# Performance work log

Hardware: AMD Instinct MI355X
Metric: run time of the kernel (lower is better)

The kernel has to match this reference:

```python
import jax, jax.numpy as jnp
import numpy as np

N = 50000      # nodes
E = 800000     # edges
DIN = 128      # input_dim
H = 128        # hidden_dim
DOUT = 64      # output_dim
G = 256        # graphs in batch
HOPS = 2       # num_hops
EPS = 1e-5     # BatchNorm eps


def setup_inputs() -> dict:
    key = jax.random.key(0)
    ks = jax.random.split(key, 16)
    w = lambda k, shape: jax.random.normal(k, shape, jnp.float32) * 0.05
    return dict(
        x=jax.random.normal(ks[0], (N, DIN), jnp.float32),
        edge_index=jax.random.randint(ks[1], (2, E), 0, N),
        batch=jnp.sort(jax.random.randint(ks[2], (N,), 0, G)),
        # preprocess FFNN (weights stored [in, out]; math == torch x @ W.T + b)
        pre_w1=w(ks[3], (DIN, H)), pre_b1=jnp.zeros((H,), jnp.float32),
        pre_w2=w(ks[4], (H, H)),   pre_b2=jnp.zeros((H,), jnp.float32),
        # per-hop GCNConv weight/bias
        conv_w=w(ks[5], (HOPS, H, H)), conv_b=jnp.zeros((HOPS, H), jnp.float32),
        # per-hop FFNN
        ffnn_w1=w(ks[6], (HOPS, H, H)), ffnn_b1=jnp.zeros((HOPS, H), jnp.float32),
        ffnn_w2=w(ks[7], (HOPS, H, H)), ffnn_b2=jnp.zeros((HOPS, H), jnp.float32),
        # per-hop BatchNorm affine params
        bn_gamma=jnp.ones((HOPS, H), jnp.float32), bn_beta=jnp.zeros((HOPS, H), jnp.float32),
        # postprocess FFNN
        post_w1=w(ks[8], (H, H)),    post_b1=jnp.zeros((H,), jnp.float32),
        post_w2=w(ks[9], (H, DOUT)), post_b2=jnp.zeros((DOUT,), jnp.float32),
    )


def _ffnn(x, w1, b1, w2, b2):
    # Linear -> GELU(exact, erf-based like nn.GELU) -> Linear
    return jax.nn.gelu(x @ w1 + b1, approximate=False) @ w2 + b2


def reference(x, edge_index, batch,
              pre_w1, pre_b1, pre_w2, pre_b2,
              conv_w, conv_b, ffnn_w1, ffnn_b1, ffnn_w2, ffnn_b2,
              bn_gamma, bn_beta,
              post_w1, post_b1, post_w2, post_b2):
    n = x.shape[0]
    loops = jnp.arange(n)
    # GCNConv default: add self-loops, symmetric D^-1/2 A D^-1/2 normalization
    src = jnp.concatenate([edge_index[0], loops])
    dst = jnp.concatenate([edge_index[1], loops])
    deg = jax.ops.segment_sum(jnp.ones(src.shape[0], x.dtype), dst, num_segments=n)
    dis = jnp.where(deg > 0, jax.lax.rsqrt(deg), 0.0)
    norm = dis[src] * dis[dst]  # [E+N]

    x = _ffnn(x, pre_w1, pre_b1, pre_w2, pre_b2)  # preprocess
    for i in range(HOPS):
        # GCNConv: (x W) gathered at src, scaled, scatter-added at dst, + bias
        xw = x @ conv_w[i]
        agg = jax.ops.segment_sum(xw[src] * norm[:, None], dst, num_segments=n) + conv_b[i]
        x = agg + x  # residual
        # BatchNorm1d (training-mode batch statistics, biased variance)
        mean = x.mean(axis=0)
        var = x.var(axis=0)
        x = (x - mean) * jax.lax.rsqrt(var + EPS) * bn_gamma[i] + bn_beta[i]
        # dropout treated as identity (deterministic reference)
        x = _ffnn(x, ffnn_w1[i], ffnn_b1[i], ffnn_w2[i], ffnn_b2[i]) + x
    # global_mean_pool over graph ids
    sums = jax.ops.segment_sum(x, batch, num_segments=G)
    cnt = jax.ops.segment_sum(jnp.ones(n, x.dtype), batch, num_segments=G)
    pooled = sums / jnp.maximum(cnt, 1.0)[:, None]
    return _ffnn(pooled, post_w1, post_b1, post_w2, post_b2)
```

## Files before the change

### kernel.cpp

```cpp
#include <hip/hip_runtime.h>
#include <hip/hip_bf16.h>
#include <math.h>

#define NN 50000
#define EE 800000
#define GG 256

typedef short bf16x8 __attribute__((ext_vector_type(8)));
typedef float f32x4 __attribute__((ext_vector_type(4)));
typedef unsigned int u32x4 __attribute__((ext_vector_type(4)));

__device__ __forceinline__ unsigned short f2bf(float x) {
    __hip_bfloat16 h = __float2bfloat16(x);
    union { __hip_bfloat16 h; unsigned short u; } c; c.h = h; return c.u;
}
__device__ __forceinline__ float bf2f(unsigned short u) {
    union { unsigned int v; float f; } t; t.v = ((unsigned int)u) << 16; return t.f;
}
__device__ __forceinline__ float gelu_f(float v) {
    return 0.5f * v * (1.0f + erff(v * 0.70710678118654752f));
}
__device__ __forceinline__ int swz(int row, int bytecol) {
    return row * 256 + (bytecol ^ ((row & 7) << 4));
}

__global__ void k_deg(const int* __restrict__ dst, int* __restrict__ degi, int E) {
    int i = blockIdx.x * blockDim.x + threadIdx.x;
    if (i < E) atomicAdd(&degi[dst[i]], 1);
}
__global__ void k_scan1(const int* __restrict__ degi, int* __restrict__ incl,
                        int* __restrict__ bsum, int N) {
    __shared__ int sm[1024];
    int t = threadIdx.x, i = blockIdx.x * 1024 + t;
    int v = (i < N) ? degi[i] : 0;
    sm[t] = v;
    __syncthreads();
    for (int off = 1; off < 1024; off <<= 1) {
        int add = (t >= off) ? sm[t - off] : 0;
        __syncthreads();
        sm[t] += add;
        __syncthreads();
    }
    if (i < N) incl[i] = sm[t];
    if (t == 1023) bsum[blockIdx.x] = sm[t];
}
__global__ void k_scan3(const int* __restrict__ incl, const int* __restrict__ degi,
                        const int* __restrict__ bsum, float* __restrict__ dis,
                        int* __restrict__ rowstart, int N, int E, int nsb) {
    __shared__ int sboff;
    int t = threadIdx.x;
    if (t < 64) {
        int nb = blockIdx.x >> 2;
        int v = (t < nb && t < nsb) ? bsum[t] : 0;
        #pragma unroll
        for (int o = 1; o < 64; o <<= 1) v += __shfl_xor(v, o, 64);
        if (t == 0) sboff = v;
    }
    __syncthreads();
    int i = blockIdx.x * 256 + t;
    if (i < N) {
        rowstart[i] = incl[i] - degi[i] + sboff;
        dis[i] = rsqrtf((float)(degi[i] + 1));
    }
    if (i == 0) rowstart[N] = E;
}
__global__ void k_fill(const int* __restrict__ src, const int* __restrict__ dst,
                       const float* __restrict__ dis, const int* __restrict__ rowstart,
                       int* __restrict__ fillc, int* __restrict__ col,
                       float* __restrict__ wn, int E) {
    int i = blockIdx.x * blockDim.x + threadIdx.x;
    if (i < E) {
        int s = src[i], d = dst[i];
        int pos = rowstart[d] + atomicAdd(&fillc[d], 1);
        col[pos] = s;
        wn[pos] = dis[s] * dis[d];
    }
}
__global__ void k_prepw8(const float* __restrict__ w0, const float* __restrict__ w1,
                         const float* __restrict__ w2, const float* __restrict__ w3,
                         const float* __restrict__ w4, const float* __restrict__ w5,
                         const float* __restrict__ w6, const float* __restrict__ w7,
                         unsigned short* __restrict__ Wt) {
    int b = blockIdx.x >> 6;
    const float* W = b == 0 ? w0 : b == 1 ? w1 : b == 2 ? w2 : b == 3 ? w3
                   : b == 4 ? w4 : b == 5 ? w5 : b == 6 ? w6 : w7;
    int tid = (blockIdx.x & 63) * 256 + threadIdx.x;
    int n = tid >> 7, k = tid & 127;
    *(unsigned short*)((char*)(Wt + (size_t)b * 16384) + swz(n, k * 2)) = f2bf(W[k * 128 + n]);
}

__global__ __launch_bounds__(256) void k_mm(
    const float* __restrict__ A32, const unsigned short* __restrict__ A16,
    const unsigned short* __restrict__ W1, const float* __restrict__ b1,
    const unsigned short* __restrict__ W2, const float* __restrict__ b2,
    const unsigned short* __restrict__ W3,
    const float* __restrict__ st_sum, const float* __restrict__ st_sq,
    const float* __restrict__ st_g, const float* __restrict__ st_b,
    float invN, int bn, int hasres,
    float* __restrict__ outx32, unsigned short* __restrict__ out3, int M)
{
    __shared__ unsigned short As[64 * 128];
    __shared__ unsigned short Ws[128 * 128];
    __shared__ float lsc[128], lsh[128];
    const int tid = threadIdx.x;
    const int bm = blockIdx.x * 64;
    if (st_sum && tid < 128) {
        float m = st_sum[tid] * invN;
        float var = st_sq[tid] * invN - m * m;
        float s = st_g[tid] * rsqrtf(var + 1e-5f);
        lsc[tid] = s;
        lsh[tid] = st_b[tid] - m * s;
    }
    __syncthreads();
    {
        const uint4* srcp = (const uint4*)W1;
        uint4* dstp = (uint4*)Ws;
        for (int i = tid; i < 2048; i += 256) dstp[i] = srcp[i];
    }
    #pragma unroll
    for (int pass = 0; pass < 4; ++pass) {
        int row = pass * 16 + (tid >> 4);
        int c8 = tid & 15;
        int gr = bm + row; if (gr > M - 1) gr = M - 1;
        float vv[8];
        if (A32) {
            const float* pp = A32 + (size_t)gr * 128 + c8 * 8;
            float4 v0 = *(const float4*)pp;
            float4 v1 = *(const float4*)(pp + 4);
            vv[0] = v0.x; vv[1] = v0.y; vv[2] = v0.z; vv[3] = v0.w;
            vv[4] = v1.x; vv[5] = v1.y; vv[6] = v1.z; vv[7] = v1.w;
        } else {
            u32x4 raw = __builtin_nontemporal_load((const u32x4*)(A16 + (size_t)gr * 128 + c8 * 8));
            #pragma unroll
            for (int d = 0; d < 4; ++d) {
                vv[2 * d]     = bf2f((unsigned short)(raw[d] & 0xffff));
                vv[2 * d + 1] = bf2f((unsigned short)(raw[d] >> 16));
            }
        }
        if (bn) {
            int ch = c8 * 8;
            #pragma unroll
            for (int j = 0; j < 8; ++j) vv[j] = vv[j] * lsc[ch + j] + lsh[ch + j];
        }
        unsigned short tmp[8];
        #pragma unroll
        for (int j = 0; j < 8; ++j) tmp[j] = f2bf(vv[j]);
        *(uint4*)((char*)As + swz(row, c8 * 16)) = *(uint4*)tmp;
    }
    __syncthreads();

    const int lane = tid & 63, wid = tid >> 6;
    const int r0 = wid * 16;
    const int lrow = lane & 15;
    const int lkb = (lane >> 4) * 16;
    const int cb = lane & 15;
    const int rb = r0 + (lane >> 4) * 4;

    f32x4 acc[8];
    #pragma unroll
    for (int n = 0; n < 8; ++n) acc[n] = (f32x4){0.f, 0.f, 0.f, 0.f};
    #pragma unroll
    for (int kk = 0; kk < 4; ++kk) {
        int bc = kk * 64 + lkb;
        bf16x8 a = *(const bf16x8*)((const char*)As + swz(r0 + lrow, bc));
        #pragma unroll
        for (int n = 0; n < 8; ++n) {
            bf16x8 b = *(const bf16x8*)((const char*)Ws + swz(n * 16 + lrow, bc));
            acc[n] = __builtin_amdgcn_mfma_f32_16x16x32_bf16(a, b, acc[n], 0, 0, 0);
        }
    }
    unsigned short rres[32];
    if (hasres) {
        #pragma unroll
        for (int n = 0; n < 8; ++n)
            #pragma unroll
            for (int j = 0; j < 4; ++j)
                rres[n * 4 + j] = *(const unsigned short*)((const char*)As + swz(rb + j, (n * 16 + cb) * 2));
    }
    #pragma unroll
    for (int n = 0; n < 8; ++n) {
        int colg = n * 16 + cb;
        float bv = b1[colg];
        #pragma unroll
        for (int j = 0; j < 4; ++j) {
            float v = gelu_f(acc[n][j] + bv);
            *(unsigned short*)((char*)As + swz(rb + j, colg * 2)) = f2bf(v);
        }
    }
    __syncthreads();
    {
        const uint4* srcp = (const uint4*)W2;
        uint4* dstp = (uint4*)Ws;
        for (int i = tid; i < 2048; i += 256) dstp[i] = srcp[i];
    }
    __syncthreads();
    #pragma unroll
    for (int n = 0; n < 8; ++n) acc[n] = (f32x4){0.f, 0.f, 0.f, 0.f};
    #pragma unroll
    for (int kk = 0; kk < 4; ++kk) {
        int bc = kk * 64 + lkb;
        bf16x8 a = *(const bf16x8*)((const char*)As + swz(r0 + lrow, bc));
        #pragma unroll
        for (int n = 0; n < 8; ++n) {
            bf16x8 b = *(const bf16x8*)((const char*)Ws + swz(n * 16 + lrow, bc));
            acc[n] = __builtin_amdgcn_mfma_f32_16x16x32_bf16(a, b, acc[n], 0, 0, 0);
        }
    }
    #pragma unroll
    for (int n = 0; n < 8; ++n) {
        int colg = n * 16 + cb;
        float bv = b2[colg];
        #pragma unroll
        for (int j = 0; j < 4; ++j) {
            int rowg = bm + rb + j;
            float v = acc[n][j] + bv;
            if (hasres) v += bf2f(rres[n * 4 + j]);
            if (rowg < M) outx32[(size_t)rowg * 128 + colg] = v;
            if (W3) *(unsigned short*)((char*)As + swz(rb + j, colg * 2)) = f2bf(v);
        }
    }
    if (!W3) return;
    __syncthreads();
    {
        const uint4* srcp = (const uint4*)W3;
        uint4* dstp = (uint4*)Ws;
        for (int i = tid; i < 2048; i += 256) dstp[i] = srcp[i];
    }
    __syncthreads();
    #pragma unroll
    for (int n = 0; n < 8; ++n) acc[n] = (f32x4){0.f, 0.f, 0.f, 0.f};
    #pragma unroll
    for (int kk = 0; kk < 4; ++kk) {
        int bc = kk * 64 + lkb;
        bf16x8 a = *(const bf16x8*)((const char*)As + swz(r0 + lrow, bc));
        #pragma unroll
        for (int n = 0; n < 8; ++n) {
            bf16x8 b = *(const bf16x8*)((const char*)Ws + swz(n * 16 + lrow, bc));
            acc[n] = __builtin_amdgcn_mfma_f32_16x16x32_bf16(a, b, acc[n], 0, 0, 0);
        }
    }
    #pragma unroll
    for (int n = 0; n < 8; ++n) {
        int colg = n * 16 + cb;
        #pragma unroll
        for (int j = 0; j < 4; ++j) {
            int rowg = bm + rb + j;
            if (rowg < M) out3[(size_t)rowg * 128 + colg] = f2bf(acc[n][j]);
        }
    }
}

__global__ __launch_bounds__(256) void k_agg(
    const unsigned short* __restrict__ xw, const int* __restrict__ rowstart,
    const int* __restrict__ col, const float* __restrict__ wn,
    const float* __restrict__ dis, const float* __restrict__ convb,
    const float* __restrict__ x0, unsigned short* __restrict__ zbf,
    float* __restrict__ bnsum, float* __restrict__ bnsq, int N)
{
    __shared__ float redS[4][128];
    __shared__ float redQ[4][128];
    const int tid = threadIdx.x;
    const int lane = tid & 63;
    const int wid = tid >> 6;
    const int g = lane >> 4;
    const int cl = lane & 15;
    const int ch = cl * 8;
    const int wave = blockIdx.x * 4 + wid;
    const int nwaves = gridDim.x * 4;

    float cb[8];
    #pragma unroll
    for (int j = 0; j < 8; ++j) cb[j] = convb[ch + j];
    float s[8], q[8];
    #pragma unroll
    for (int j = 0; j < 8; ++j) { s[j] = 0.f; q[j] = 0.f; }

    for (int v = wave; v < N; v += nwaves) {
        const int e0 = rowstart[v], e1 = rowstart[v + 1];
        float a[8];
        #pragma unroll
        for (int j = 0; j < 8; ++j) a[j] = 0.f;
        int e = e0 + g;
        for (; e + 4 < e1; e += 8) {
            const int u0 = __builtin_nontemporal_load(col + e);
            const float w0 = __builtin_nontemporal_load(wn + e);
            const int u1 = __builtin_nontemporal_load(col + e + 4);
            const float w1 = __builtin_nontemporal_load(wn + e + 4);
            u32x4 p0 = *(const u32x4*)(xw + (size_t)u0 * 128 + ch);
            u32x4 p1 = *(const u32x4*)(xw + (size_t)u1 * 128 + ch);
            #pragma unroll
            for (int d = 0; d < 4; ++d) {
                a[2 * d]     += w0 * bf2f((unsigned short)(p0[d] & 0xffff));
                a[2 * d + 1] += w0 * bf2f((unsigned short)(p0[d] >> 16));
            }
            #pragma unroll
            for (int d = 0; d < 4; ++d) {
                a[2 * d]     += w1 * bf2f((unsigned short)(p1[d] & 0xffff));
                a[2 * d + 1] += w1 * bf2f((unsigned short)(p1[d] >> 16));
            }
        }
        if (e < e1) {
            const int u = __builtin_nontemporal_load(col + e);
            const float w = __builtin_nontemporal_load(wn + e);
            u32x4 p = *(const u32x4*)(xw + (size_t)u * 128 + ch);
            #pragma unroll
            for (int d = 0; d < 4; ++d) {
                a[2 * d]     += w * bf2f((unsigned short)(p[d] & 0xffff));
                a[2 * d + 1] += w * bf2f((unsigned short)(p[d] >> 16));
            }
        }
        #pragma unroll
        for (int j = 0; j < 8; ++j) {
            a[j] += __shfl_xor(a[j], 16, 64);
            a[j] += __shfl_xor(a[j], 32, 64);
        }
        if (g == 0) {
            const float dv = dis[v];
            const float sw = dv * dv;
            u32x4 p = *(const u32x4*)(xw + (size_t)v * 128 + ch);
            f32x4 xa = __builtin_nontemporal_load((const f32x4*)(x0 + (size_t)v * 128 + ch));
            f32x4 xb = __builtin_nontemporal_load((const f32x4*)(x0 + (size_t)v * 128 + ch + 4));
            const float xr[8] = { xa[0], xa[1], xa[2], xa[3], xb[0], xb[1], xb[2], xb[3] };
            float zz[8];
            #pragma unroll
            for (int d = 0; d < 4; ++d) {
                zz[2 * d]     = a[2 * d]     + sw * bf2f((unsigned short)(p[d] & 0xffff));
                zz[2 * d + 1] = a[2 * d + 1] + sw * bf2f((unsigned short)(p[d] >> 16));
            }
            unsigned short zo[8];
            #pragma unroll
            for (int j = 0; j < 8; ++j) {
                zz[j] += cb[j] + xr[j];
                s[j] += zz[j];
                q[j] += zz[j] * zz[j];
                zo[j] = f2bf(zz[j]);
            }
            __builtin_nontemporal_store(*(const u32x4*)zo, (u32x4*)(zbf + (size_t)v * 128 + ch));
        }
    }
    if (g == 0) {
        #pragma unroll
        for (int j = 0; j < 8; ++j) { redS[wid][ch + j] = s[j]; redQ[wid][ch + j] = q[j]; }
    }
    __syncthreads();
    if (tid < 128) {
        float ts = redS[0][tid] + redS[1][tid] + redS[2][tid] + redS[3][tid];
        float tq = redQ[0][tid] + redQ[1][tid] + redQ[2][tid] + redQ[3][tid];
        atomicAdd(&bnsum[tid], ts);
        atomicAdd(&bnsq[tid], tq);
    }
}
__global__ __launch_bounds__(128) void k_pool(
    const float* __restrict__ x, const int* __restrict__ batch,
    float* __restrict__ pooled, int* __restrict__ cnt, int N)
{
    const int t = threadIdx.x;
    const int per = (N + gridDim.x - 1) / gridDim.x;
    const int s = blockIdx.x * per;
    const int e = min(s + per, N);
    if (s >= e) return;
    float acc = 0.f;
    int gcur = batch[s];
    int run = 0;
    for (int v = s; v < e; ++v) {
        int g = batch[v];
        if (g != gcur) {
            atomicAdd(&pooled[(size_t)gcur * 128 + t], acc);
            if (t == 0) atomicAdd(&cnt[gcur], run);
            acc = 0.f; run = 0; gcur = g;
        }
        acc += __builtin_nontemporal_load(x + (size_t)v * 128 + t);
        ++run;
    }
    atomicAdd(&pooled[(size_t)gcur * 128 + t], acc);
    if (t == 0) atomicAdd(&cnt[gcur], run);
}
__global__ __launch_bounds__(128) void k_post(
    const float* __restrict__ pooled, const int* __restrict__ cnt,
    const float* __restrict__ w1, const float* __restrict__ b1,
    const float* __restrict__ w2, const float* __restrict__ b2,
    float* __restrict__ out, int G)
{
    __shared__ float pr[128], hr[128];
    int g = blockIdx.x, t = threadIdx.x;
    float c = fmaxf((float)cnt[g], 1.0f);
    pr[t] = pooled[(size_t)g * 128 + t] / c;
    __syncthreads();
    float a = b1[t];
    for (int k = 0; k < 128; ++k) a += pr[k] * w1[k * 128 + t];
    hr[t] = gelu_f(a);
    __syncthreads();
    if (t < 64) {
        float o = b2[t];
        for (int k = 0; k < 128; ++k) o += hr[k] * w2[k * 64 + t];
        out[g * 64 + t] = o;
    }
}

extern "C" void kernel_launch(void* const* d_in, const int* in_sizes, int n_in,
                              void* d_out, int out_size, void* d_ws, size_t ws_size,
                              hipStream_t stream) {
    (void)in_sizes; (void)n_in; (void)out_size; (void)ws_size;
    const float* x_in    = (const float*)d_in[0];
    const int*   ei      = (const int*)d_in[1];
    const int*   batch   = (const int*)d_in[2];
    const float* pre_w1  = (const float*)d_in[3];
    const float* pre_b1  = (const float*)d_in[4];
    const float* pre_w2  = (const float*)d_in[5];
    const float* pre_b2  = (const float*)d_in[6];
    const float* conv_w  = (const float*)d_in[7];
    const float* conv_b  = (const float*)d_in[8];
    const float* ffnn_w1 = (const float*)d_in[9];
    const float* ffnn_b1 = (const float*)d_in[10];
    const float* ffnn_w2 = (const float*)d_in[11];
    const float* ffnn_b2 = (const float*)d_in[12];
    const float* bn_gamma= (const float*)d_in[13];
    const float* bn_beta = (const float*)d_in[14];
    const float* post_w1 = (const float*)d_in[15];
    const float* post_b1 = (const float*)d_in[16];
    const float* post_w2 = (const float*)d_in[17];
    const float* post_b2 = (const float*)d_in[18];
    const int* srcE = ei;
    const int* dstE = ei + EE;

    char* base = (char*)d_ws;
    size_t off = 0;
    auto carve = [&](size_t bytes) {
        char* q = base + off;
        off = (off + bytes + 255) & ~(size_t)255;
        return q;
    };
    float* xf32 = (float*)carve((size_t)NN * 128 * 4);
    unsigned short* zbf = (unsigned short*)carve((size_t)NN * 128 * 2);
    unsigned short* hbf = (unsigned short*)carve((size_t)NN * 128 * 2);
    float* dis   = (float*)carve((size_t)NN * 4);
    int*   degi  = (int*)carve((size_t)NN * 4);
    int*   fillc = (int*)carve((size_t)NN * 4);
    float* pooled= (float*)carve((size_t)GG * 128 * 4);
    int*   cnt   = (int*)carve((size_t)GG * 4);
    float* bnstat= (float*)carve(512 * 4);
    size_t zlen  = (size_t)((char*)(bnstat + 512) - (char*)degi);
    int* incl    = (int*)carve((size_t)NN * 4);
    int* bsum    = (int*)carve(64 * 4);
    int* rowstart= (int*)carve((size_t)(NN + 1) * 4);
    int* colx    = (int*)carve((size_t)EE * 4);
    float* wn    = (float*)carve((size_t)EE * 4);
    unsigned short* Wt = (unsigned short*)carve((size_t)8 * 16384 * 2);

    hipMemsetAsync(degi, 0, zlen, stream);

    const int nsb = (NN + 1023) / 1024;
    k_deg<<<(EE + 255) / 256, 256, 0, stream>>>(dstE, degi, EE);
    k_scan1<<<nsb, 1024, 0, stream>>>(degi, incl, bsum, NN);
    k_scan3<<<(NN + 255) / 256, 256, 0, stream>>>(incl, degi, bsum, dis, rowstart, NN, EE, nsb);
    k_fill<<<(EE + 255) / 256, 256, 0, stream>>>(srcE, dstE, dis, rowstart, fillc, colx, wn, EE);
    k_prepw8<<<512, 256, 0, stream>>>(pre_w1, pre_w2, conv_w, conv_w + 16384,
                                      ffnn_w1, ffnn_w1 + 16384, ffnn_w2, ffnn_w2 + 16384, Wt);

    const int gB = (NN + 63) / 64;
    const float invN = 1.0f / NN;
    k_mm<<<gB, 256, 0, stream>>>(x_in, nullptr, Wt + 0 * 16384, pre_b1, Wt + 1 * 16384, pre_b2,
                                 Wt + 2 * 16384, nullptr, nullptr, nullptr, nullptr,
                                 invN, 0, 0, xf32, hbf, NN);
    k_agg<<<2048, 256, 0, stream>>>(hbf, rowstart, colx, wn, dis, conv_b,
                                    xf32, zbf, bnstat, bnstat + 128, NN);
    k_mm<<<gB, 256, 0, stream>>>(nullptr, zbf, Wt + 4 * 16384, ffnn_b1, Wt + 6 * 16384, ffnn_b2,
                                 Wt + 3 * 16384, bnstat, bnstat + 128, bn_gamma, bn_beta,
                                 invN, 1, 1, xf32, hbf, NN);
    k_agg<<<2048, 256, 0, stream>>>(hbf, rowstart, colx, wn, dis, conv_b + 128,
                                    xf32, zbf, bnstat + 256, bnstat + 384, NN);
    k_mm<<<gB, 256, 0, stream>>>(nullptr, zbf, Wt + 5 * 16384, ffnn_b1 + 128, Wt + 7 * 16384, ffnn_b2 + 128,
                                 nullptr, bnstat + 256, bnstat + 384, bn_gamma + 128, bn_beta + 128,
                                 invN, 1, 1, xf32, nullptr, NN);
    k_pool<<<1024, 128, 0, stream>>>(xf32, batch, pooled, cnt, NN);
    k_post<<<GG, 128, 0, stream>>>(pooled, cnt, post_w1, post_b1, post_w2, post_b2,
                                   (float*)d_out, GG);
}
```

Measured before the change: 396.6 us.

## Fold GCN normalization into node scaling and fuse mean-pool into final FFNN

The symmetric normalization is refactored: the xW output is pre-scaled by dis[src] in the matmul epilogue and the aggregate is scaled by dis[dst] once per node. This removes the per-edge weight array and its loads, and k_agg gains a 4-way unrolled gather loop. The final FFNN kernel now accumulates graph sums directly into pooled via shared memory and atomics, which drops the fp32 x write and the separate pool kernel. Graph counts come from a binary search over the sorted batch array. The trade-off is bf16 rounding of the pre-scaled values and a dependence on batch being sorted.

```diff
diff --git a/kernel.cpp b/kernel.cpp
--- a/kernel.cpp
+++ b/kernel.cpp
@@ -65,15 +65,13 @@
     if (i == 0) rowstart[N] = E;
 }
 __global__ void k_fill(const int* __restrict__ src, const int* __restrict__ dst,
-                       const float* __restrict__ dis, const int* __restrict__ rowstart,
-                       int* __restrict__ fillc, int* __restrict__ col,
-                       float* __restrict__ wn, int E) {
+                       const int* __restrict__ rowstart,
+                       int* __restrict__ fillc, int* __restrict__ col, int E) {
     int i = blockIdx.x * blockDim.x + threadIdx.x;
     if (i < E) {
         int s = src[i], d = dst[i];
         int pos = rowstart[d] + atomicAdd(&fillc[d], 1);
         col[pos] = s;
-        wn[pos] = dis[s] * dis[d];
     }
 }
 __global__ void k_prepw8(const float* __restrict__ w0, const float* __restrict__ w1,
@@ -93,15 +91,18 @@
     const float* __restrict__ A32, const unsigned short* __restrict__ A16,
     const unsigned short* __restrict__ W1, const float* __restrict__ b1,
     const unsigned short* __restrict__ W2, const float* __restrict__ b2,
-    const unsigned short* __restrict__ W3,
+    const unsigned short* __restrict__ W3, const float* __restrict__ disv,
     const float* __restrict__ st_sum, const float* __restrict__ st_sq,
     const float* __restrict__ st_g, const float* __restrict__ st_b,
     float invN, int bn, int hasres,
-    float* __restrict__ outx32, unsigned short* __restrict__ out3, int M)
+    float* __restrict__ outx32, unsigned short* __restrict__ out3,
+    const int* __restrict__ batch, float* __restrict__ pooled, int M)
 {
     __shared__ unsigned short As[64 * 128];
     __shared__ unsigned short Ws[128 * 128];
     __shared__ float lsc[128], lsh[128];
+    __shared__ float sdis[64];
+    __shared__ int gid[64];
     const int tid = threadIdx.x;
     const int bm = blockIdx.x * 64;
     if (st_sum && tid < 128) {
@@ -206,6 +207,8 @@
             acc[n] = __builtin_amdgcn_mfma_f32_16x16x32_bf16(a, b, acc[n], 0, 0, 0);
         }
     }
+    const int dopool = (pooled != nullptr);
+    float* wsf = (float*)Ws;
     #pragma unroll
     for (int n = 0; n < 8; ++n) {
         int colg = n * 16 + cb;
@@ -215,9 +218,29 @@
             int rowg = bm + rb + j;
             float v = acc[n][j] + bv;
             if (hasres) v += bf2f(rres[n * 4 + j]);
-            if (rowg < M) outx32[(size_t)rowg * 128 + colg] = v;
+            if (outx32 && rowg < M) outx32[(size_t)rowg * 128 + colg] = v;
             if (W3) *(unsigned short*)((char*)As + swz(rb + j, colg * 2)) = f2bf(v);
-        }
+            if (dopool) wsf[(rb + j) * 128 + colg] = v;
+        }
+    }
+    if (dopool) {
+        if (tid < 64) { int r = bm + tid; gid[tid] = (r < M) ? batch[r] : -1; }
+        __syncthreads();
+        if (tid < 128) {
+            float pacc = 0.f;
+            int gcur = gid[0];
+            #pragma unroll 4
+            for (int r = 0; r < 64; ++r) {
+                int gg = gid[r];
+                if (gg != gcur) {
+                    if (gcur >= 0) atomicAdd(&pooled[(size_t)gcur * 128 + tid], pacc);
+                    pacc = 0.f; gcur = gg;
+                }
+                if (gg >= 0) pacc += wsf[r * 128 + tid];
+            }
+            if (gcur >= 0) atomicAdd(&pooled[(size_t)gcur * 128 + tid], pacc);
+        }
+        return;
     }
     if (!W3) return;
     __syncthreads();
@@ -225,6 +248,7 @@
         const uint4* srcp = (const uint4*)W3;
         uint4* dstp = (uint4*)Ws;
         for (int i = tid; i < 2048; i += 256) dstp[i] = srcp[i];
+        if (tid < 64) { int r = bm + tid; sdis[tid] = disv[(r < M) ? r : (M - 1)]; }
     }
     __syncthreads();
     #pragma unroll
@@ -245,14 +269,14 @@
         #pragma unroll
         for (int j = 0; j < 4; ++j) {
             int rowg = bm + rb + j;
-            if (rowg < M) out3[(size_t)rowg * 128 + colg] = f2bf(acc[n][j]);
+            if (rowg < M) out3[(size_t)rowg * 128 + colg] = f2bf(acc[n][j] * sdis[rb + j]);
         }
     }
 }
 
 __global__ __launch_bounds__(256) void k_agg(
-    const unsigned short* __restrict__ xw, const int* __restrict__ rowstart,
-    const int* __restrict__ col, const float* __restrict__ wn,
+    const unsigned short* __restrict__ xws, const int* __restrict__ rowstart,
+    const int* __restrict__ col,
     const float* __restrict__ dis, const float* __restrict__ convb,
     const float* __restrict__ x0, unsigned short* __restrict__ zbf,
     float* __restrict__ bnsum, float* __restrict__ bnsq, int N)
@@ -281,32 +305,41 @@
         #pragma unroll
         for (int j = 0; j < 8; ++j) a[j] = 0.f;
         int e = e0 + g;
+        for (; e + 12 < e1; e += 16) {
+            const int u0 = col[e];
+            const int u1 = col[e + 4];
+            const int u2 = col[e + 8];
+            const int u3 = col[e + 12];
+            u32x4 p0 = *(const u32x4*)(xws + (size_t)u0 * 128 + ch);
+            u32x4 p1 = *(const u32x4*)(xws + (size_t)u1 * 128 + ch);
+            u32x4 p2 = *(const u32x4*)(xws + (size_t)u2 * 128 + ch);
+            u32x4 p3 = *(const u32x4*)(xws + (size_t)u3 * 128 + ch);
+            #pragma unroll
+            for (int d = 0; d < 4; ++d) {
+                a[2 * d]     += bf2f((unsigned short)(p0[d] & 0xffff)) + bf2f((unsigned short)(p1[d] & 0xffff))
+                              + bf2f((unsigned short)(p2[d] & 0xffff)) + bf2f((unsigned short)(p3[d] & 0xffff));
+                a[2 * d + 1] += bf2f((unsigned short)(p0[d] >> 16)) + bf2f((unsigned short)(p1[d] >> 16))
+                              + bf2f((unsigned short)(p2[d] >> 16)) + bf2f((unsigned short)(p3[d] >> 16));
+            }
+        }
         for (; e + 4 < e1; e += 8) {
-            const int u0 = __builtin_nontemporal_load(col + e);
-            const float w0 = __builtin_nontemporal_load(wn + e);
-            const int u1 = __builtin_nontemporal_load(col + e + 4);
-            const float w1 = __builtin_nontemporal_load(wn + e + 4);
-            u32x4 p0 = *(const u32x4*)(xw + (size_t)u0 * 128 + ch);
-            u32x4 p1 = *(const u32x4*)(xw + (size_t)u1 * 128 + ch);
+            const int u0 = col[e];
+            const int u1 = col[e + 4];
+            u32x4 p0 = *(const u32x4*)(xws + (size_t)u0 * 128 + ch);
+            u32x4 p1 = *(const u32x4*)(xws + (size_t)u1 * 128 + ch);
             #pragma unroll
             for (int d = 0; d < 4; ++d) {
-                a[2 * d]     += w0 * bf2f((unsigned short)(p0[d] & 0xffff));
-                a[2 * d + 1] += w0 * bf2f((unsigned short)(p0[d] >> 16));
-            }
+                a[2 * d]     += bf2f((unsigned short)(p0[d] & 0xffff)) + bf2f((unsigned short)(p1[d] & 0xffff));
+                a[2 * d + 1] += bf2f((unsigned short)(p0[d] >> 16)) + bf2f((unsigned short)(p1[d] >> 16));
+            }
+        }
+        if (e < e1) {
+            const int u = col[e];
+            u32x4 p = *(const u32x4*)(xws + (size_t)u * 128 + ch);
             #pragma unroll
             for (int d = 0; d < 4; ++d) {
-                a[2 * d]     += w1 * bf2f((unsigned short)(p1[d] & 0xffff));
-                a[2 * d + 1] += w1 * bf2f((unsigned short)(p1[d] >> 16));
-            }
-        }
-        if (e < e1) {
-            const int u = __builtin_nontemporal_load(col + e);
-            const float w = __builtin_nontemporal_load(wn + e);
-            u32x4 p = *(const u32x4*)(xw + (size_t)u * 128 + ch);
-            #pragma unroll
-            for (int d = 0; d < 4; ++d) {
-                a[2 * d]     += w * bf2f((unsigned short)(p[d] & 0xffff));
-                a[2 * d + 1] += w * bf2f((unsigned short)(p[d] >> 16));
+                a[2 * d]     += bf2f((unsigned short)(p[d] & 0xffff));
+                a[2 * d + 1] += bf2f((unsigned short)(p[d] >> 16));
             }
         }
         #pragma unroll
@@ -316,16 +349,15 @@
         }
         if (g == 0) {
             const float dv = dis[v];
-            const float sw = dv * dv;
-            u32x4 p = *(const u32x4*)(xw + (size_t)v * 128 + ch);
+            u32x4 p = *(const u32x4*)(xws + (size_t)v * 128 + ch);
             f32x4 xa = __builtin_nontemporal_load((const f32x4*)(x0 + (size_t)v * 128 + ch));
             f32x4 xb = __builtin_nontemporal_load((const f32x4*)(x0 + (size_t)v * 128 + ch + 4));
             const float xr[8] = { xa[0], xa[1], xa[2], xa[3], xb[0], xb[1], xb[2], xb[3] };
             float zz[8];
             #pragma unroll
             for (int d = 0; d < 4; ++d) {
-                zz[2 * d]     = a[2 * d]     + sw * bf2f((unsigned short)(p[d] & 0xffff));
-                zz[2 * d + 1] = a[2 * d + 1] + sw * bf2f((unsigned short)(p[d] >> 16));
+                zz[2 * d]     = dv * (a[2 * d]     + bf2f((unsigned short)(p[d] & 0xffff)));
+                zz[2 * d + 1] = dv * (a[2 * d + 1] + bf2f((unsigned short)(p[d] >> 16)));
             }
             unsigned short zo[8];
             #pragma unroll
@@ -350,40 +382,22 @@
         atomicAdd(&bnsq[tid], tq);
     }
 }
-__global__ __launch_bounds__(128) void k_pool(
-    const float* __restrict__ x, const int* __restrict__ batch,
-    float* __restrict__ pooled, int* __restrict__ cnt, int N)
-{
-    const int t = threadIdx.x;
-    const int per = (N + gridDim.x - 1) / gridDim.x;
-    const int s = blockIdx.x * per;
-    const int e = min(s + per, N);
-    if (s >= e) return;
-    float acc = 0.f;
-    int gcur = batch[s];
-    int run = 0;
-    for (int v = s; v < e; ++v) {
-        int g = batch[v];
-        if (g != gcur) {
-            atomicAdd(&pooled[(size_t)gcur * 128 + t], acc);
-            if (t == 0) atomicAdd(&cnt[gcur], run);
-            acc = 0.f; run = 0; gcur = g;
-        }
-        acc += __builtin_nontemporal_load(x + (size_t)v * 128 + t);
-        ++run;
-    }
-    atomicAdd(&pooled[(size_t)gcur * 128 + t], acc);
-    if (t == 0) atomicAdd(&cnt[gcur], run);
-}
 __global__ __launch_bounds__(128) void k_post(
-    const float* __restrict__ pooled, const int* __restrict__ cnt,
+    const float* __restrict__ pooled, const int* __restrict__ batch,
     const float* __restrict__ w1, const float* __restrict__ b1,
     const float* __restrict__ w2, const float* __restrict__ b2,
-    float* __restrict__ out, int G)
+    float* __restrict__ out, int N, int G)
 {
     __shared__ float pr[128], hr[128];
+    __shared__ int bounds[2];
     int g = blockIdx.x, t = threadIdx.x;
-    float c = fmaxf((float)cnt[g], 1.0f);
+    if (t < 2) {
+        int tgt = g + t, lo = 0, hi = N;
+        while (lo < hi) { int mid = (lo + hi) >> 1; if (batch[mid] < tgt) lo = mid + 1; else hi = mid; }
+        bounds[t] = lo;
+    }
+    __syncthreads();
+    float c = fmaxf((float)(bounds[1] - bounds[0]), 1.0f);
     pr[t] = pooled[(size_t)g * 128 + t] / c;
     __syncthreads();
     float a = b1[t];
@@ -437,14 +451,12 @@
     int*   degi  = (int*)carve((size_t)NN * 4);
     int*   fillc = (int*)carve((size_t)NN * 4);
     float* pooled= (float*)carve((size_t)GG * 128 * 4);
-    int*   cnt   = (int*)carve((size_t)GG * 4);
     float* bnstat= (float*)carve(512 * 4);
     size_t zlen  = (size_t)((char*)(bnstat + 512) - (char*)degi);
     int* incl    = (int*)carve((size_t)NN * 4);
     int* bsum    = (int*)carve(64 * 4);
     int* rowstart= (int*)carve((size_t)(NN + 1) * 4);
     int* colx    = (int*)carve((size_t)EE * 4);
-    float* wn    = (float*)carve((size_t)EE * 4);
     unsigned short* Wt = (unsigned short*)carve((size_t)8 * 16384 * 2);
 
     hipMemsetAsync(degi, 0, zlen, stream);
@@ -453,26 +465,25 @@
     k_deg<<<(EE + 255) / 256, 256, 0, stream>>>(dstE, degi, EE);
     k_scan1<<<nsb, 1024, 0, stream>>>(degi, incl, bsum, NN);
     k_scan3<<<(NN + 255) / 256, 256, 0, stream>>>(incl, degi, bsum, dis, rowstart, NN, EE, nsb);
-    k_fill<<<(EE + 255) / 256, 256, 0, stream>>>(srcE, dstE, dis, rowstart, fillc, colx, wn, EE);
+    k_fill<<<(EE + 255) / 256, 256, 0, stream>>>(srcE, dstE, rowstart, fillc, colx, EE);
     k_prepw8<<<512, 256, 0, stream>>>(pre_w1, pre_w2, conv_w, conv_w + 16384,
                                       ffnn_w1, ffnn_w1 + 16384, ffnn_w2, ffnn_w2 + 16384, Wt);
 
     const int gB = (NN + 63) / 64;
     const float invN = 1.0f / NN;
     k_mm<<<gB, 256, 0, stream>>>(x_in, nullptr, Wt + 0 * 16384, pre_b1, Wt + 1 * 16384, pre_b2,
-                                 Wt + 2 * 16384, nullptr, nullptr, nullptr, nullptr,
-                                 invN, 0, 0, xf32, hbf, NN);
-    k_agg<<<2048, 256, 0, stream>>>(hbf, rowstart, colx, wn, dis, conv_b,
+                                 Wt + 2 * 16384, dis, nullptr, nullptr, nullptr, nullptr,
+                                 invN, 0, 0, xf32, hbf, nullptr, nullptr, NN);
+    k_agg<<<2048, 256, 0, stream>>>(hbf, rowstart, colx, dis, conv_b,
                                     xf32, zbf, bnstat, bnstat + 128, NN);
     k_mm<<<gB, 256, 0, stream>>>(nullptr, zbf, Wt + 4 * 16384, ffnn_b1, Wt + 6 * 16384, ffnn_b2,
-                                 Wt + 3 * 16384, bnstat, bnstat + 128, bn_gamma, bn_beta,
-                                 invN, 1, 1, xf32, hbf, NN);
-    k_agg<<<2048, 256, 0, stream>>>(hbf, rowstart, colx, wn, dis, conv_b + 128,
+                                 Wt + 3 * 16384, dis, bnstat, bnstat + 128, bn_gamma, bn_beta,
+                                 invN, 1, 1, xf32, hbf, nullptr, nullptr, NN);
+    k_agg<<<2048, 256, 0, stream>>>(hbf, rowstart, colx, dis, conv_b + 128,
                                     xf32, zbf, bnstat + 256, bnstat + 384, NN);
     k_mm<<<gB, 256, 0, stream>>>(nullptr, zbf, Wt + 5 * 16384, ffnn_b1 + 128, Wt + 7 * 16384, ffnn_b2 + 128,
-                                 nullptr, bnstat + 256, bnstat + 384, bn_gamma + 128, bn_beta + 128,
-                                 invN, 1, 1, xf32, nullptr, NN);
-    k_pool<<<1024, 128, 0, stream>>>(xf32, batch, pooled, cnt, NN);
-    k_post<<<GG, 128, 0, stream>>>(pooled, cnt, post_w1, post_b1, post_w2, post_b2,
-                                   (float*)d_out, GG);
-}
+                                 nullptr, nullptr, bnstat + 256, bnstat + 384, bn_gamma + 128, bn_beta + 128,
+                                 invN, 1, 1, nullptr, nullptr, batch, pooled, NN);
+    k_post<<<GG, 128, 0, stream>>>(pooled, batch, post_w1, post_b1, post_w2, post_b2,
+                                   (float*)d_out, NN, GG);
+}
```

Result: faster. 381.9 us (-3.7%).
